# Kernel tuning notes

Measured on AMD Instinct MI355X. Metric: run time of the kernel, lower is better.

## Reference

```python
import jax, jax.numpy as jnp
import numpy as np
import math

D_MODEL = 768
NHEAD = 12
D_HEAD = D_MODEL // NHEAD
TAU = 300.0
NEG = -1e9

def setup_inputs() -> dict:
    key = jax.random.key(0)
    ks = jax.random.split(key, 12)
    N, L, D = 64, 512, D_MODEL
    tokens = jax.random.normal(ks[0], (N, L, D), dtype=jnp.float32)
    ts = jax.random.uniform(ks[1], (N, L, 1), dtype=jnp.float32) * 3600.0  # seconds in a 1h window
    mask = jnp.ones((N, L, 1), dtype=jnp.float32)
    s = 1.0 / math.sqrt(D)
    Wq = jax.random.normal(ks[2], (D, D), dtype=jnp.float32) * s
    bq = jnp.zeros((D,), dtype=jnp.float32)
    Wk = jax.random.normal(ks[3], (D, D), dtype=jnp.float32) * s
    bk = jnp.zeros((D,), dtype=jnp.float32)
    Wv = jax.random.normal(ks[4], (D, D), dtype=jnp.float32) * s
    bv = jnp.zeros((D,), dtype=jnp.float32)
    Wo = jax.random.normal(ks[5], (D, D), dtype=jnp.float32) * s
    bo = jnp.zeros((D,), dtype=jnp.float32)
    readout = jax.random.normal(ks[6], (1, 1, D), dtype=jnp.float32)
    return dict(tokens=tokens, ts=ts, mask=mask, Wq=Wq, bq=bq, Wk=Wk, bk=bk,
                Wv=Wv, bv=bv, Wo=Wo, bo=bo, readout=readout)

def _heads(x, N, L):
    return x.reshape(N, L, NHEAD, D_HEAD).transpose(0, 2, 1, 3)  # (N,H,L,dh)

def reference(tokens, ts, mask, Wq, bq, Wk, bk, Wv, bv, Wo, bo, readout):
    N, L, D = tokens.shape
    scale = 1.0 / math.sqrt(D_HEAD)
    # time-decay bias: log(exp(-|dt|/tau) + 1e-12)
    t = (ts - ts[:, :1, :])[..., 0]                       # (N,L)
    dt = jnp.abs(t[:, :, None] - t[:, None, :])           # (N,L,L)
    bias = jnp.log(jnp.exp(-dt / max(TAU, 1e-6)) + 1e-12)
    q = _heads(tokens @ Wq.T + bq, N, L)
    k = _heads(tokens @ Wk.T + bk, N, L)
    v = _heads(tokens @ Wv.T + bv, N, L)
    attn = jnp.einsum('nhqd,nhkd->nhqk', q, k) * scale + bias[:, None, :, :]
    key_pad = mask[..., 0] <= 0                           # (N,L)
    attn = jnp.where(key_pad[:, None, None, :], NEG, attn)
    A = jax.nn.softmax(attn, axis=-1)
    out = jnp.einsum('nhqk,nhkd->nhqd', A, v).transpose(0, 2, 1, 3).reshape(N, L, D)
    out = (out @ Wo.T + bo) * mask
    # readout pooling attention (single learned query)
    qh = jnp.broadcast_to(readout, (N, 1, D)).reshape(N, 1, NHEAD, D_HEAD).transpose(0, 2, 1, 3)
    kh = _heads(out, N, L)
    pool = jnp.einsum('nhqd,nhkd->nhqk', qh, kh) * scale  # (N,H,1,L)
    pool = jnp.where(key_pad[:, None, None, :], NEG, pool)
    P = jax.nn.softmax(pool, axis=-1)
    pooled = jnp.einsum('nhqk,nhkd->nhqd', P, kh).transpose(0, 2, 1, 3).reshape(N, 1, D)
    return pooled[:, 0, :]
```

## Files before the change

kernel.cpp:

```cpp
#include <hip/hip_runtime.h>
#include <stdint.h>

#define AS1 __attribute__((address_space(1)))
#define AS3 __attribute__((address_space(3)))

typedef __bf16 bf16x8 __attribute__((ext_vector_type(8)));
typedef float  f32x4  __attribute__((ext_vector_type(4)));
typedef float  f32x16 __attribute__((ext_vector_type(16)));

#define MFMA16(a, b, c) __builtin_amdgcn_mfma_f32_16x16x32_bf16((a), (b), (c), 0, 0, 0)
#define MFMA32(a, b, c) __builtin_amdgcn_mfma_f32_32x32x16_bf16((a), (b), (c), 0, 0, 0)

#define SEQ   512
#define NBAT  64
#define DM    768
#define NH    12
#define DH    64
#define NQKV  2304
#define NTOK  (NBAT * SEQ)
#define NKB   12

__device__ __forceinline__ uint16_t f2bf(float x) {
  uint32_t u = __float_as_uint(x);
  return (uint16_t)((u + 0x7FFFu + ((u >> 16) & 1u)) >> 16);
}

__device__ __forceinline__ void async16(uint16_t* lds, const uint16_t* g) {
  __builtin_amdgcn_global_load_lds((AS1 void*)(uintptr_t)(const void*)g,
                                   (AS3 void*)lds, 16, 0, 0);
}

__device__ __forceinline__ int swz(int r) { return (r ^ (r >> 3)) & 7; }

__global__ __launch_bounds__(256) void k_cvt(
    const float* __restrict__ tokens,
    const float* __restrict__ Wq, const float* __restrict__ Wk,
    const float* __restrict__ Wv, const float* __restrict__ Wo,
    const float* __restrict__ bq, const float* __restrict__ bk, const float* __restrict__ bv,
    uint16_t* __restrict__ X, uint16_t* __restrict__ Wqkv_pk, uint16_t* __restrict__ Wob_pk,
    float* __restrict__ bqkv) {
  int i = blockIdx.x * 256 + threadIdx.x;
  {
    const float4* sp = (const float4*)tokens;
    float4 a = sp[2 * i], b = sp[2 * i + 1];
    union { uint16_t u[8]; uint4 v; } o;
    o.u[0] = f2bf(a.x); o.u[1] = f2bf(a.y); o.u[2] = f2bf(a.z); o.u[3] = f2bf(a.w);
    o.u[4] = f2bf(b.x); o.u[5] = f2bf(b.y); o.u[6] = f2bf(b.z); o.u[7] = f2bf(b.w);
    ((uint4*)X)[i] = o.v;
  }
  if (i < 221184) {
    int lane = i & 63, ks = (i >> 6) & 3, kb = (i >> 8) % NKB, g = i / 3072;
    int row = g * 32 + (lane & 31);
    int k   = kb * 64 + ks * 16 + (lane >> 5) * 8;
    const float* src = (row < 768)  ? Wq + (size_t)row * 768 + k
                     : (row < 1536) ? Wk + (size_t)(row - 768) * 768 + k
                                    : Wv + (size_t)(row - 1536) * 768 + k;
    float4 a = *(const float4*)src, b = *(const float4*)(src + 4);
    union { uint16_t u[8]; uint4 v; } o;
    o.u[0] = f2bf(a.x); o.u[1] = f2bf(a.y); o.u[2] = f2bf(a.z); o.u[3] = f2bf(a.w);
    o.u[4] = f2bf(b.x); o.u[5] = f2bf(b.y); o.u[6] = f2bf(b.z); o.u[7] = f2bf(b.w);
    ((uint4*)Wqkv_pk)[i] = o.v;
  }
  if (i < 73728) {
    int lane = i & 63, ks = (i >> 6) & 3, kb = (i >> 8) % NKB, g = i / 3072;
    int row = g * 32 + (lane & 31);
    int k   = kb * 64 + ks * 16 + (lane >> 5) * 8;
    const float* src = Wo + (size_t)row * 768 + k;
    float4 a = *(const float4*)src, b = *(const float4*)(src + 4);
    union { uint16_t u[8]; uint4 v; } o;
    o.u[0] = f2bf(a.x); o.u[1] = f2bf(a.y); o.u[2] = f2bf(a.z); o.u[3] = f2bf(a.w);
    o.u[4] = f2bf(b.x); o.u[5] = f2bf(b.y); o.u[6] = f2bf(b.z); o.u[7] = f2bf(b.w);
    ((uint4*)Wob_pk)[i] = o.v;
  }
  if (i < 768) { bqkv[i] = bq[i]; bqkv[i + 768] = bk[i]; bqkv[i + 1536] = bv[i]; }
}

__global__ __launch_bounds__(256, 4) void k_gemm_bt(
    const uint16_t* __restrict__ A, const uint16_t* __restrict__ Bpk,
    const float* __restrict__ bias, const float* __restrict__ rowscale,
    uint16_t* __restrict__ C, int ldc, int ncol) {
  __shared__ uint16_t Alds[128 * 64];
  const int tid  = threadIdx.x;
  const int w    = tid >> 6, lane = tid & 63;
  const int wu   = __builtin_amdgcn_readfirstlane(w);
  const int l32  = lane & 31, kh = lane >> 5;
  const int sup  = blockIdx.x / (32 * ncol);
  const int t    = blockIdx.x % (32 * ncol);
  const int row0 = (sup * 32 + (t & 31)) * 128, col0 = (t >> 5) * 128;
  const int wrow = (w >> 1) * 64,   wcol = (w & 1) * 64;

  const uint16_t* bw = Bpk + (size_t)((col0 >> 5) + (w & 1) * 2) * (NKB * 2048) + lane * 8;

  f32x16 acc[2][2] = {};
  for (int kb = 0; kb < NKB; ++kb) {
    __syncthreads();
#pragma unroll
    for (int j = 0; j < 4; ++j) {
      int cid = j * 256 + w * 64 + lane;
      int r = cid >> 3, cc = cid & 7, c = cc ^ swz(r);
      async16(&Alds[(j * 256 + wu * 64) * 8],
              A + (size_t)(row0 + r) * 768 + kb * 64 + c * 8);
    }
    __syncthreads();
#pragma unroll
    for (int ks = 0; ks < 4; ++ks) {
      bf16x8 bfr[2];
#pragma unroll
      for (int nt = 0; nt < 2; ++nt)
        bfr[nt] = *(const bf16x8*)(bw + (size_t)nt * (NKB * 2048) + (kb * 4 + ks) * 512);
      bf16x8 af[2];
#pragma unroll
      for (int mt = 0; mt < 2; ++mt) {
        int r = wrow + mt * 32 + l32;
        int c = (ks * 2 + kh) ^ swz(r);
        af[mt] = *(const bf16x8*)&Alds[r * 64 + c * 8];
      }
#pragma unroll
      for (int mt = 0; mt < 2; ++mt)
#pragma unroll
        for (int nt = 0; nt < 2; ++nt)
          acc[mt][nt] = MFMA32(af[mt], bfr[nt], acc[mt][nt]);
    }
  }
#pragma unroll
  for (int nt = 0; nt < 2; ++nt) {
    int col = col0 + wcol + nt * 32 + l32;
    float bv = bias[col];
#pragma unroll
    for (int mt = 0; mt < 2; ++mt) {
#pragma unroll
      for (int rg = 0; rg < 16; ++rg) {
        int row = row0 + wrow + mt * 32 + (rg & 3) + 8 * (rg >> 2) + 4 * kh;
        float v = acc[mt][nt][rg] + bv;
        if (rowscale) v *= rowscale[row];
        C[(size_t)row * ldc + col] = f2bf(v);
      }
    }
  }
}

__global__ __launch_bounds__(512) void k_attn(
    const uint16_t* __restrict__ QKV, const float* __restrict__ ts,
    const float* __restrict__ mask, uint16_t* __restrict__ Aout) {
  __shared__ uint16_t Klds[2][64 * 64];
  __shared__ uint16_t Vt[64 * 72];
  __shared__ uint16_t Plds[8][2 * 32 * 40];
  __shared__ float tkl[SEQ];

  const int tid = threadIdx.x, w = tid >> 6, lane = tid & 63;
  const int wu = __builtin_amdgcn_readfirstlane(w);
  const int quad = lane >> 4, l16 = lane & 15;
  int b = blockIdx.x;
  int xcd = b & 7, i = b >> 3;
  int qtp = i & 1;
  int hg = xcd * 96 + (i >> 1);
  int n = hg / NH, h = hg % NH;
  const int q0 = (qtp * 2 + (w >> 2)) * 128 + (w & 3) * 32;
  const size_t rowbase = (size_t)n * SEQ * NQKV;

  const float c1 = 0.125f * 1.44269504f;
  const float c2 = 1.44269504f / 300.0f;

  for (int l = tid; l < SEQ; l += 512) {
    float t = ts[n * SEQ + l] * c2;
    tkl[l] = (mask[n * SEQ + l] > 0.f) ? t : 3e38f;
  }

  bf16x8 qf[2][2];
  float tq[2][4];
#pragma unroll
  for (int qs = 0; qs < 2; ++qs) {
    int qr = q0 + qs * 16 + l16;
    const uint16_t* qp = QKV + rowbase + (size_t)qr * NQKV + h * DH;
#pragma unroll
    for (int dsp = 0; dsp < 2; ++dsp)
      qf[qs][dsp] = *(const bf16x8*)(qp + dsp * 32 + quad * 8);
#pragma unroll
    for (int rg = 0; rg < 4; ++rg)
      tq[qs][rg] = ts[n * SEQ + q0 + qs * 16 + quad * 4 + rg] * c2;
  }

  f32x4 accO[2][4] = {};
  f32x4 accL[2] = {};
  bf16x8 ones_b;
  {
    union { uint16_t u[8]; bf16x8 v; } t;
    uint16_t o = (l16 == 0) ? 0x3F80 : 0;
#pragma unroll
    for (int j = 0; j < 8; ++j) t.u[j] = o;
    ones_b = t.v;
  }
  uint16_t* Pw = &Plds[w][0];

  const uint16_t* Kbase = QKV + rowbase + DM + h * DH;
  const uint16_t* Vbase = QKV + rowbase + 2 * DM + h * DH;
  const int vr = tid & 63, vdb = (tid >> 6) * 8;
  const int kr = tid >> 3, kc = (tid & 7) ^ swz(tid >> 3);
  uint4 vreg0;

  async16(&Klds[0][wu * 64 * 8], Kbase + (size_t)kr * NQKV + kc * 8);
  vreg0 = *(const uint4*)(Vbase + (size_t)vr * NQKV + vdb);
  __syncthreads();
  {
    union { uint4 v; uint16_t u[8]; } a0;
    a0.v = vreg0;
#pragma unroll
    for (int j = 0; j < 8; ++j) Vt[(vdb + j) * 72 + vr] = a0.u[j];
  }
  __syncthreads();

  for (int it = 0; it < 8; ++it) {
    const int k0 = it * 64, cur = it & 1;
    if (it < 7) {
      async16(&Klds[cur ^ 1][wu * 64 * 8],
              Kbase + (size_t)(k0 + 64 + kr) * NQKV + kc * 8);
      vreg0 = *(const uint4*)(Vbase + (size_t)(k0 + 64 + vr) * NQKV + vdb);
    }

#pragma unroll
    for (int kt = 0; kt < 2; ++kt) {
      uint16_t* Pk = Pw + kt * 1280;
      f32x4 s[2][2] = {};
      __builtin_amdgcn_s_setprio(1);
#pragma unroll
      for (int dsp = 0; dsp < 2; ++dsp) {
        bf16x8 kf[2];
#pragma unroll
        for (int ksu = 0; ksu < 2; ++ksu) {
          int r = kt * 32 + 2 * l16 + ksu;
          int c = (dsp * 4 + quad) ^ swz(r);
          kf[ksu] = *(const bf16x8*)&Klds[cur][r * 64 + c * 8];
        }
#pragma unroll
        for (int qs = 0; qs < 2; ++qs)
#pragma unroll
          for (int ksu = 0; ksu < 2; ++ksu)
            s[qs][ksu] = MFMA16(qf[qs][dsp], kf[ksu], s[qs][ksu]);
      }
      __builtin_amdgcn_s_setprio(0);
      float tk0 = tkl[k0 + kt * 32 + 2 * l16];
      float tk1 = tkl[k0 + kt * 32 + 2 * l16 + 1];
#pragma unroll
      for (int qs = 0; qs < 2; ++qs) {
#pragma unroll
        for (int rg = 0; rg < 4; ++rg) {
          float d0 = fabsf(tq[qs][rg] - tk0);
          float d1 = fabsf(tq[qs][rg] - tk1);
          float p0 = __builtin_amdgcn_exp2f(fmaf(s[qs][0][rg], c1, -d0));
          float p1 = __builtin_amdgcn_exp2f(fmaf(s[qs][1][rg], c1, -d1));
          uint32_t u = (__float_as_uint(p0) >> 16) | (__float_as_uint(p1) & 0xFFFF0000u);
          *(uint32_t*)(Pk + (qs * 16 + quad * 4 + rg) * 40 + 2 * l16) = u;
        }
      }
      bf16x8 vb[4];
#pragma unroll
      for (int dt = 0; dt < 4; ++dt)
        vb[dt] = *(const bf16x8*)&Vt[(dt * 16 + l16) * 72 + kt * 32 + quad * 8];
      __builtin_amdgcn_s_setprio(1);
#pragma unroll
      for (int qs = 0; qs < 2; ++qs) {
        bf16x8 pa = *(const bf16x8*)(Pk + (qs * 16 + l16) * 40 + quad * 8);
#pragma unroll
        for (int dt = 0; dt < 4; ++dt)
          accO[qs][dt] = MFMA16(pa, vb[dt], accO[qs][dt]);
        accL[qs] = MFMA16(pa, ones_b, accL[qs]);
      }
      __builtin_amdgcn_s_setprio(0);
    }

    __syncthreads();
    if (it < 7) {
      union { uint4 v; uint16_t u[8]; } a0;
      a0.v = vreg0;
#pragma unroll
      for (int j = 0; j < 8; ++j) Vt[(vdb + j) * 72 + vr] = a0.u[j];
    }
    __syncthreads();
  }
#pragma unroll
  for (int qs = 0; qs < 2; ++qs) {
    float inv[4];
#pragma unroll
    for (int rg = 0; rg < 4; ++rg) {
      float lv = __shfl(accL[qs][rg], lane & 48, 64);
      inv[rg] = 1.0f / lv;
    }
#pragma unroll
    for (int dt = 0; dt < 4; ++dt) {
#pragma unroll
      for (int rg = 0; rg < 4; ++rg) {
        int qr = q0 + qs * 16 + quad * 4 + rg;
        float v = accO[qs][dt][rg] * inv[rg];
        Aout[(size_t)(n * SEQ + qr) * DM + h * DH + dt * 16 + l16] = f2bf(v);
      }
    }
  }
}

__global__ __launch_bounds__(256) void k_pool(
    const uint16_t* __restrict__ Out, const float* __restrict__ mask,
    const float* __restrict__ readout, float* __restrict__ dst) {
  __shared__ float rsl[64];
  __shared__ float ex[SEQ];
  __shared__ float red[4];
  __shared__ float part[8][64];
  int b = blockIdx.x;
  int n = b / NH, h = b % NH;
  int tid = threadIdx.x;
  if (tid < 64) rsl[tid] = readout[h * DH + tid];
  __syncthreads();

  float suml = 0.f;
  for (int l = tid; l < SEQ; l += 256) {
    const uint16_t* rowp = Out + (size_t)(n * SEQ + l) * DM + h * DH;
    float acc = 0.f;
#pragma unroll
    for (int c = 0; c < 8; ++c) {
      union { uint4 v; uint16_t u[8]; } t;
      t.v = *(const uint4*)(rowp + c * 8);
#pragma unroll
      for (int j = 0; j < 8; ++j)
        acc += __uint_as_float(((uint32_t)t.u[j]) << 16) * rsl[c * 8 + j];
    }
    float e = __builtin_amdgcn_exp2f(acc * (0.125f * 1.44269504f));
    e = (mask[n * SEQ + l] > 0.f) ? e : 0.f;
    ex[l] = e;
    suml += e;
  }
#pragma unroll
  for (int off = 32; off; off >>= 1) suml += __shfl_down(suml, off, 64);
  if ((tid & 63) == 0) red[tid >> 6] = suml;
  __syncthreads();
  float inv = 1.0f / (red[0] + red[1] + red[2] + red[3]);

  int d0 = (tid & 31) * 2, ch = tid >> 5;
  float a0 = 0.f, a1 = 0.f;
  for (int l = ch * 64; l < ch * 64 + 64; ++l) {
    uint32_t pv = *(const uint32_t*)(Out + (size_t)(n * SEQ + l) * DM + h * DH + d0);
    float e = ex[l];
    a0 = fmaf(__uint_as_float(pv << 16), e, a0);
    a1 = fmaf(__uint_as_float(pv & 0xFFFF0000u), e, a1);
  }
  part[ch][d0] = a0;
  part[ch][d0 + 1] = a1;
  __syncthreads();
  if (tid < 64) {
    float s = 0.f;
#pragma unroll
    for (int c = 0; c < 8; ++c) s += part[c][tid];
    dst[n * DM + h * DH + tid] = s * inv;
  }
}

extern "C" void kernel_launch(void* const* d_in, const int* in_sizes, int n_in,
                              void* d_out, int out_size, void* d_ws, size_t ws_size,
                              hipStream_t stream) {
  const float* tokens  = (const float*)d_in[0];
  const float* ts      = (const float*)d_in[1];
  const float* mask    = (const float*)d_in[2];
  const float* Wq      = (const float*)d_in[3];
  const float* bq      = (const float*)d_in[4];
  const float* Wk      = (const float*)d_in[5];
  const float* bk      = (const float*)d_in[6];
  const float* Wv      = (const float*)d_in[7];
  const float* bv      = (const float*)d_in[8];
  const float* Wo      = (const float*)d_in[9];
  const float* bo      = (const float*)d_in[10];
  const float* readout = (const float*)d_in[11];

  char* ws = (char*)d_ws;
  uint16_t* X    = (uint16_t*)ws;
  uint16_t* Wqkv = (uint16_t*)(ws + 50331648);
  uint16_t* Wob  = (uint16_t*)(ws + 53870592);
  float*    bqkv = (float*)   (ws + 55050240);
  uint16_t* QKV  = (uint16_t*)(ws + 55059456);
  uint16_t* attn = X;
  uint16_t* Outb = QKV;

  k_cvt<<<12288, 256, 0, stream>>>(tokens, Wq, Wk, Wv, Wo, bq, bk, bv, X, Wqkv, Wob, bqkv);
  k_gemm_bt<<<4608, 256, 0, stream>>>(X, Wqkv, bqkv, nullptr, QKV, NQKV, 18);
  k_attn<<<1536, 512, 0, stream>>>(QKV, ts, mask, attn);
  k_gemm_bt<<<1536, 256, 0, stream>>>(attn, Wob, bo, mask, Outb, DM, 6);
  k_pool<<<768, 256, 0, stream>>>(Outb, mask, readout, (float*)d_out);
}
```

Baseline: 468.2 us.

## Compute transposed S=K·Q^T in attention, pass P via lane shuffles instead of LDS

The attention kernel now computes the score tile transposed so each lane holds one query column. The exp'd probabilities are packed into the PV MFMA operand with cross-lane shuffles rather than a round trip through per-wave LDS. The row sum is accumulated in registers instead of with an extra MFMA against a ones vector. V is double-buffered in LDS, which removes one __syncthreads per iteration, and output stores become 8-byte vector writes. The changes aim to cut LDS traffic, barriers and MFMA count, at the cost of more shuffles and higher register pressure, with a launch bound of 4 blocks per CU.

Measured after the change: 607.2 us. 1.3x slower.

```diff
diff --git a/kernel.cpp b/kernel.cpp
--- a/kernel.cpp
+++ b/kernel.cpp
@@ -139,12 +139,11 @@
   }
 }
 
-__global__ __launch_bounds__(512) void k_attn(
+__global__ __launch_bounds__(512, 4) void k_attn(
     const uint16_t* __restrict__ QKV, const float* __restrict__ ts,
     const float* __restrict__ mask, uint16_t* __restrict__ Aout) {
   __shared__ uint16_t Klds[2][64 * 64];
-  __shared__ uint16_t Vt[64 * 72];
-  __shared__ uint16_t Plds[8][2 * 32 * 40];
+  __shared__ uint16_t Vt[2][64 * 72];
   __shared__ float tkl[SEQ];
 
   const int tid = threadIdx.x, w = tid >> 6, lane = tid & 63;
@@ -167,7 +166,7 @@
   }
 
   bf16x8 qf[2][2];
-  float tq[2][4];
+  float tq[2];
 #pragma unroll
   for (int qs = 0; qs < 2; ++qs) {
     int qr = q0 + qs * 16 + l16;
@@ -175,27 +174,18 @@
 #pragma unroll
     for (int dsp = 0; dsp < 2; ++dsp)
       qf[qs][dsp] = *(const bf16x8*)(qp + dsp * 32 + quad * 8);
-#pragma unroll
-    for (int rg = 0; rg < 4; ++rg)
-      tq[qs][rg] = ts[n * SEQ + q0 + qs * 16 + quad * 4 + rg] * c2;
+    tq[qs] = ts[n * SEQ + qr] * c2;
   }
 
   f32x4 accO[2][4] = {};
-  f32x4 accL[2] = {};
-  bf16x8 ones_b;
-  {
-    union { uint16_t u[8]; bf16x8 v; } t;
-    uint16_t o = (l16 == 0) ? 0x3F80 : 0;
-#pragma unroll
-    for (int j = 0; j < 8; ++j) t.u[j] = o;
-    ones_b = t.v;
-  }
-  uint16_t* Pw = &Plds[w][0];
+  float accL[2] = {0.f, 0.f};
 
   const uint16_t* Kbase = QKV + rowbase + DM + h * DH;
   const uint16_t* Vbase = QKV + rowbase + 2 * DM + h * DH;
   const int vr = tid & 63, vdb = (tid >> 6) * 8;
   const int kr = tid >> 3, kc = (tid & 7) ^ swz(tid >> 3);
+  const int sA = l16 + ((quad & 1) << 5);
+  const int sB = sA + 16;
   uint4 vreg0;
 
   async16(&Klds[0][wu * 64 * 8], Kbase + (size_t)kr * NQKV + kc * 8);
@@ -205,7 +195,7 @@
     union { uint4 v; uint16_t u[8]; } a0;
     a0.v = vreg0;
 #pragma unroll
-    for (int j = 0; j < 8; ++j) Vt[(vdb + j) * 72 + vr] = a0.u[j];
+    for (int j = 0; j < 8; ++j) Vt[0][(vdb + j) * 72 + vr] = a0.u[j];
   }
   __syncthreads();
 
@@ -219,80 +209,90 @@
 
 #pragma unroll
     for (int kt = 0; kt < 2; ++kt) {
-      uint16_t* Pk = Pw + kt * 1280;
       f32x4 s[2][2] = {};
       __builtin_amdgcn_s_setprio(1);
 #pragma unroll
       for (int dsp = 0; dsp < 2; ++dsp) {
-        bf16x8 kf[2];
-#pragma unroll
-        for (int ksu = 0; ksu < 2; ++ksu) {
-          int r = kt * 32 + 2 * l16 + ksu;
+        bf16x8 kfA[2];
+#pragma unroll
+        for (int km = 0; km < 2; ++km) {
+          int r = kt * 32 + km * 16 + l16;
           int c = (dsp * 4 + quad) ^ swz(r);
-          kf[ksu] = *(const bf16x8*)&Klds[cur][r * 64 + c * 8];
+          kfA[km] = *(const bf16x8*)&Klds[cur][r * 64 + c * 8];
         }
 #pragma unroll
         for (int qs = 0; qs < 2; ++qs)
 #pragma unroll
-          for (int ksu = 0; ksu < 2; ++ksu)
-            s[qs][ksu] = MFMA16(qf[qs][dsp], kf[ksu], s[qs][ksu]);
+          for (int km = 0; km < 2; ++km)
+            s[qs][km] = MFMA16(kfA[km], qf[qs][dsp], s[qs][km]);
       }
       __builtin_amdgcn_s_setprio(0);
-      float tk0 = tkl[k0 + kt * 32 + 2 * l16];
-      float tk1 = tkl[k0 + kt * 32 + 2 * l16 + 1];
+
+      float4 tka = *(const float4*)&tkl[k0 + kt * 32 + quad * 4];
+      float4 tkb = *(const float4*)&tkl[k0 + kt * 32 + 16 + quad * 4];
+
+      bf16x8 vb[4];
+#pragma unroll
+      for (int dt = 0; dt < 4; ++dt)
+        vb[dt] = *(const bf16x8*)&Vt[cur][(dt * 16 + l16) * 72 + kt * 32 + quad * 8];
+
 #pragma unroll
       for (int qs = 0; qs < 2; ++qs) {
-#pragma unroll
-        for (int rg = 0; rg < 4; ++rg) {
-          float d0 = fabsf(tq[qs][rg] - tk0);
-          float d1 = fabsf(tq[qs][rg] - tk1);
-          float p0 = __builtin_amdgcn_exp2f(fmaf(s[qs][0][rg], c1, -d0));
-          float p1 = __builtin_amdgcn_exp2f(fmaf(s[qs][1][rg], c1, -d1));
-          uint32_t u = (__float_as_uint(p0) >> 16) | (__float_as_uint(p1) & 0xFFFF0000u);
-          *(uint32_t*)(Pk + (qs * 16 + quad * 4 + rg) * 40 + 2 * l16) = u;
-        }
+        float tqv = tq[qs];
+        float p00 = __builtin_amdgcn_exp2f(fmaf(s[qs][0][0], c1, -fabsf(tqv - tka.x)));
+        float p01 = __builtin_amdgcn_exp2f(fmaf(s[qs][0][1], c1, -fabsf(tqv - tka.y)));
+        float p02 = __builtin_amdgcn_exp2f(fmaf(s[qs][0][2], c1, -fabsf(tqv - tka.z)));
+        float p03 = __builtin_amdgcn_exp2f(fmaf(s[qs][0][3], c1, -fabsf(tqv - tka.w)));
+        float p10 = __builtin_amdgcn_exp2f(fmaf(s[qs][1][0], c1, -fabsf(tqv - tkb.x)));
+        float p11 = __builtin_amdgcn_exp2f(fmaf(s[qs][1][1], c1, -fabsf(tqv - tkb.y)));
+        float p12 = __builtin_amdgcn_exp2f(fmaf(s[qs][1][2], c1, -fabsf(tqv - tkb.z)));
+        float p13 = __builtin_amdgcn_exp2f(fmaf(s[qs][1][3], c1, -fabsf(tqv - tkb.w)));
+        accL[qs] += (p00 + p01 + p02 + p03) + (p10 + p11 + p12 + p13);
+        uint32_t w00 = (__float_as_uint(p00) >> 16) | (__float_as_uint(p01) & 0xFFFF0000u);
+        uint32_t w01 = (__float_as_uint(p02) >> 16) | (__float_as_uint(p03) & 0xFFFF0000u);
+        uint32_t w10 = (__float_as_uint(p10) >> 16) | (__float_as_uint(p11) & 0xFFFF0000u);
+        uint32_t w11 = (__float_as_uint(p12) >> 16) | (__float_as_uint(p13) & 0xFFFF0000u);
+        uint32_t a0 = __shfl(w00, sA, 64), a1 = __shfl(w01, sA, 64);
+        uint32_t b0 = __shfl(w00, sB, 64), b1 = __shfl(w01, sB, 64);
+        uint32_t c0 = __shfl(w10, sA, 64), c1r = __shfl(w11, sA, 64);
+        uint32_t d0 = __shfl(w10, sB, 64), d1 = __shfl(w11, sB, 64);
+        bool lo = quad < 2;
+        union { uint32_t u[4]; bf16x8 v; } pa;
+        pa.u[0] = lo ? a0 : c0;
+        pa.u[1] = lo ? a1 : c1r;
+        pa.u[2] = lo ? b0 : d0;
+        pa.u[3] = lo ? b1 : d1;
+        __builtin_amdgcn_s_setprio(1);
+#pragma unroll
+        for (int dt = 0; dt < 4; ++dt)
+          accO[qs][dt] = MFMA16(vb[dt], pa.v, accO[qs][dt]);
+        __builtin_amdgcn_s_setprio(0);
       }
-      bf16x8 vb[4];
-#pragma unroll
-      for (int dt = 0; dt < 4; ++dt)
-        vb[dt] = *(const bf16x8*)&Vt[(dt * 16 + l16) * 72 + kt * 32 + quad * 8];
-      __builtin_amdgcn_s_setprio(1);
-#pragma unroll
-      for (int qs = 0; qs < 2; ++qs) {
-        bf16x8 pa = *(const bf16x8*)(Pk + (qs * 16 + l16) * 40 + quad * 8);
-#pragma unroll
-        for (int dt = 0; dt < 4; ++dt)
-          accO[qs][dt] = MFMA16(pa, vb[dt], accO[qs][dt]);
-        accL[qs] = MFMA16(pa, ones_b, accL[qs]);
-      }
-      __builtin_amdgcn_s_setprio(0);
-    }
-
-    __syncthreads();
+    }
+
     if (it < 7) {
       union { uint4 v; uint16_t u[8]; } a0;
       a0.v = vreg0;
 #pragma unroll
-      for (int j = 0; j < 8; ++j) Vt[(vdb + j) * 72 + vr] = a0.u[j];
+      for (int j = 0; j < 8; ++j) Vt[cur ^ 1][(vdb + j) * 72 + vr] = a0.u[j];
     }
     __syncthreads();
   }
+
 #pragma unroll
   for (int qs = 0; qs < 2; ++qs) {
-    float inv[4];
-#pragma unroll
-    for (int rg = 0; rg < 4; ++rg) {
-      float lv = __shfl(accL[qs][rg], lane & 48, 64);
-      inv[rg] = 1.0f / lv;
-    }
+    float l = accL[qs];
+    l += __shfl_xor(l, 16, 64);
+    l += __shfl_xor(l, 32, 64);
+    float inv = 1.0f / l;
+    int qr = q0 + qs * 16 + l16;
+    uint16_t* op = Aout + (size_t)(n * SEQ + qr) * DM + h * DH + quad * 4;
 #pragma unroll
     for (int dt = 0; dt < 4; ++dt) {
-#pragma unroll
-      for (int rg = 0; rg < 4; ++rg) {
-        int qr = q0 + qs * 16 + quad * 4 + rg;
-        float v = accO[qs][dt][rg] * inv[rg];
-        Aout[(size_t)(n * SEQ + qr) * DM + h * DH + dt * 16 + l16] = f2bf(v);
-      }
+      union { uint16_t u[4]; uint2 d; } o;
+#pragma unroll
+      for (int rg = 0; rg < 4; ++rg) o.u[rg] = f2bf(accO[qs][dt][rg] * inv);
+      *(uint2*)(op + dt * 16) = o.d;
     }
   }
 }
```
